# Kernel tuning notes

Hardware: AMD Instinct MI355X
Metric: run time of the kernel (lower is better)

Reference implementation:

```python
import jax, jax.numpy as jnp
import numpy as np

NUM_EXPERTS = 8
TOP_K = 2


def setup_inputs() -> dict:
    key = jax.random.key(0)
    k1, k2, k3, k4, k5 = jax.random.split(key, 5)
    H, F, E = 1024, 4096, NUM_EXPERTS
    s = 0.02
    return {
        "hidden_states": jax.random.normal(k1, (2, 2048, H), jnp.float32),
        "w_router": jax.random.normal(k2, (E, H), jnp.float32) * s,
        "w1": jax.random.normal(k3, (E, F, H), jnp.float32) * s,
        "w2": jax.random.normal(k4, (E, H, F), jnp.float32) * s,
        "w3": jax.random.normal(k5, (E, F, H), jnp.float32) * s,
    }


def reference(hidden_states, w_router, w1, w2, w3):
    B, S, H = hidden_states.shape
    x = hidden_states.reshape(-1, H)  # [T, H]
    T = x.shape[0]
    # router (nn.Linear, no bias): logits = x @ W^T
    router_logits = x @ w_router.T  # [T, E]
    probs = jax.nn.softmax(router_logits.astype(jnp.float32), axis=-1)
    top_w, top_e = jax.lax.top_k(probs, TOP_K)  # [T, K]
    top_w = top_w / jnp.sum(top_w, axis=-1, keepdims=True)
    top_w = top_w.astype(x.dtype)
    # dense per-token gate matrix [T, E]; zero where expert not selected
    gates = jnp.zeros((T, NUM_EXPERTS), x.dtype).at[
        jnp.arange(T)[:, None], top_e
    ].add(top_w)
    out = jnp.zeros_like(x)
    for e in range(NUM_EXPERTS):  # fixed small expert loop
        h = jax.nn.silu(x @ w1[e].T) * (x @ w3[e].T)  # [T, F]
        out = out + gates[:, e:e + 1] * (h @ w2[e].T)
    return out.reshape(B, S, H), router_logits
```

## Files before the change

kernel.cpp:

```cpp
#include <hip/hip_runtime.h>
#include <hip/hip_bf16.h>
#include <stdint.h>

#define T_TOK 4096
#define H_DIM 1024
#define F_DIM 4096
#define NE 8
#define MG_BLKS 40

typedef float    f32x4  __attribute__((ext_vector_type(4)));
typedef __bf16   bf16x8 __attribute__((ext_vector_type(8)));
typedef uint16_t u16x8  __attribute__((ext_vector_type(8)));

#define AS1 __attribute__((address_space(1)))
#define AS3 __attribute__((address_space(3)))

__device__ __forceinline__ uint16_t f2bf(float f) {
  return __builtin_bit_cast(uint16_t, __float2bfloat16(f));
}

__device__ __forceinline__ void gld16(const void* g, void* l) {
  __builtin_amdgcn_global_load_lds((const AS1 void*)g, (AS3 void*)l, 16, 0, 0);
}

__global__ __launch_bounds__(256) void router_k(
    const float* __restrict__ x, const float* __restrict__ wr,
    float* __restrict__ logits, uint16_t* __restrict__ xb,
    int* __restrict__ pairTok, float* __restrict__ pairGate,
    int* __restrict__ tokSlot, int* __restrict__ cnt)
{
  const int lane = threadIdx.x & 63;
  const int wid  = threadIdx.x >> 6;
  const int t    = blockIdx.x * 4 + wid;

  const float* xp = x + (size_t)t * H_DIM + lane * 16;
  f32x4 xv[4];
#pragma unroll
  for (int i = 0; i < 4; ++i) xv[i] = *(const f32x4*)(xp + 4 * i);

  u16x8 o0, o1;
#pragma unroll
  for (int j = 0; j < 4; ++j) {
    o0[j] = f2bf(xv[0][j]); o0[j + 4] = f2bf(xv[1][j]);
    o1[j] = f2bf(xv[2][j]); o1[j + 4] = f2bf(xv[3][j]);
  }
  uint16_t* xbp = xb + (size_t)t * H_DIM + lane * 16;
  *(u16x8*)xbp       = o0;
  *(u16x8*)(xbp + 8) = o1;

  float s[NE];
#pragma unroll
  for (int e = 0; e < NE; ++e) {
    const float* wp = wr + e * H_DIM + lane * 16;
    float acc = 0.f;
#pragma unroll
    for (int i = 0; i < 4; ++i) {
      f32x4 wv = *(const f32x4*)(wp + 4 * i);
#pragma unroll
      for (int j = 0; j < 4; ++j) acc += xv[i][j] * wv[j];
    }
#pragma unroll
    for (int off = 32; off > 0; off >>= 1) acc += __shfl_xor(acc, off, 64);
    s[e] = acc;
  }

  if (lane == 0) {
#pragma unroll
    for (int e = 0; e < NE; ++e) logits[t * NE + e] = s[e];
    int e1 = 0;
#pragma unroll
    for (int e = 1; e < NE; ++e) if (s[e] > s[e1]) e1 = e;
    int e2 = (e1 == 0) ? 1 : 0;
#pragma unroll
    for (int e = 0; e < NE; ++e)
      if (e != e1 && e != e2 && s[e] > s[e2]) e2 = e;
    const float d  = s[e2] - s[e1];
    const float g1 = 1.f / (1.f + __expf(d));
    const float g2 = 1.f - g1;
    int i1 = atomicAdd(cnt + e1, 1);
    pairTok[e1 * T_TOK + i1] = t;  pairGate[e1 * T_TOK + i1] = g1;
    int i2 = atomicAdd(cnt + e2, 1);
    pairTok[e2 * T_TOK + i2] = t;  pairGate[e2 * T_TOK + i2] = g2;
    int4 sl; sl.x = e1; sl.y = i1; sl.z = e2; sl.w = i2;
    ((int4*)tokSlot)[t] = sl;
  }
}

__global__ void prefix_k(const int* __restrict__ cnt, int* __restrict__ base) {
  if (threadIdx.x == 0) {
    int b = 0;
#pragma unroll
    for (int e = 0; e < NE; ++e) { base[e] = b; b += (cnt[e] + 255) & ~255; }
    base[NE] = b;
  }
}

__global__ __launch_bounds__(256, 2) void ffn1_k(
    const uint16_t* __restrict__ xb, const float* __restrict__ w1,
    const float* __restrict__ w3, uint16_t* __restrict__ hbuf,
    const int* __restrict__ pairTok, const float* __restrict__ pairGate,
    const int* __restrict__ cnt, const int* __restrict__ base)
{
  const int mg0 = blockIdx.y * 256;
  if (mg0 >= base[NE]) return;
  int e = 0;
#pragma unroll
  for (int k = 1; k < NE; ++k) if (mg0 >= base[k]) e = k;
  const int m0   = mg0 - base[e];
  const int cnte = cnt[e];
  const int n0   = blockIdx.x * 64;
  const int tid  = threadIdx.x;
  const int lane = tid & 63;
  const int wid  = tid >> 6;
  const int wm   = (wid >> 1) * 128;
  const int wn   = (wid & 1) * 32;

  __shared__ __align__(16) uint16_t lsA [256 * 64];
  __shared__ __align__(16) uint16_t lsB1[ 64 * 64];
  __shared__ __align__(16) uint16_t lsB3[ 64 * 64];
  __shared__ float lsG[256];

  {
    const int rr = m0 + tid;
    lsG[tid] = (rr < cnte) ? pairGate[e * T_TOK + rr] : 0.f;
  }

  const float* w1e = w1 + (size_t)e * F_DIM * H_DIM;
  const float* w3e = w3 + (size_t)e * F_DIM * H_DIM;

  const uint16_t* asrc[8];
#pragma unroll
  for (int q = 0; q < 8; ++q) {
    const int c = q * 256 + tid;
    const int row = c >> 3, pos = c & 7;
    const int kc  = pos ^ (row & 7);
    int ar = m0 + row; if (ar >= cnte) ar = cnte - 1;
    const int tok = pairTok[e * T_TOK + ar];
    asrc[q] = xb + (size_t)tok * H_DIM + kc * 8;
  }
  const float* b1src[2];
  const float* b3src[2];
  int bdst[2];
#pragma unroll
  for (int q = 0; q < 2; ++q) {
    const int c = q * 256 + tid;
    const int row = c >> 3, pos = c & 7;
    const int kc  = pos ^ (row & 7);
    bdst[q] = c * 8;
    b1src[q] = w1e + (size_t)(n0 + row) * H_DIM + kc * 8;
    b3src[q] = w3e + (size_t)(n0 + row) * H_DIM + kc * 8;
  }

  const f32x4 fz = {0.f, 0.f, 0.f, 0.f};
  f32x4 acc1[8][2], acc3[8][2];
#pragma unroll
  for (int i = 0; i < 8; ++i)
#pragma unroll
    for (int j = 0; j < 2; ++j) { acc1[i][j] = fz; acc3[i][j] = fz; }

  for (int kt = 0; kt < H_DIM; kt += 64) {
    __syncthreads();
#pragma unroll
    for (int q = 0; q < 8; ++q)
      gld16(asrc[q] + kt, &lsA[(q * 256 + tid) * 8]);
#pragma unroll
    for (int q = 0; q < 2; ++q) {
      const float* s1 = b1src[q] + kt;
      const float* s3 = b3src[q] + kt;
      f32x4 a0 = *(const f32x4*)s1;
      f32x4 a1 = *(const f32x4*)(s1 + 4);
      f32x4 c0 = *(const f32x4*)s3;
      f32x4 c1 = *(const f32x4*)(s3 + 4);
      u16x8 ob1, ob3;
#pragma unroll
      for (int j = 0; j < 4; ++j) {
        ob1[j] = f2bf(a0[j]); ob1[j + 4] = f2bf(a1[j]);
        ob3[j] = f2bf(c0[j]); ob3[j + 4] = f2bf(c1[j]);
      }
      *(u16x8*)&lsB1[bdst[q]] = ob1;
      *(u16x8*)&lsB3[bdst[q]] = ob3;
    }
    __syncthreads();
#pragma unroll
    for (int ks = 0; ks < 2; ++ks) {
      const int kg = ks * 4 + (lane >> 4);
      bf16x8 af[8], b1f[2], b3f[2];
#pragma unroll
      for (int i = 0; i < 8; ++i) {
        const int ar = wm + i * 16 + (lane & 15);
        af[i] = *(const bf16x8*)&lsA[ar * 64 + ((kg ^ (ar & 7)) * 8)];
      }
#pragma unroll
      for (int j = 0; j < 2; ++j) {
        const int br = wn + j * 16 + (lane & 15);
        b1f[j] = *(const bf16x8*)&lsB1[br * 64 + ((kg ^ (br & 7)) * 8)];
        b3f[j] = *(const bf16x8*)&lsB3[br * 64 + ((kg ^ (br & 7)) * 8)];
      }
#pragma unroll
      for (int i = 0; i < 8; ++i)
#pragma unroll
        for (int j = 0; j < 2; ++j) {
          acc1[i][j] = __builtin_amdgcn_mfma_f32_16x16x32_bf16(af[i], b1f[j], acc1[i][j], 0, 0, 0);
          acc3[i][j] = __builtin_amdgcn_mfma_f32_16x16x32_bf16(af[i], b3f[j], acc3[i][j], 0, 0, 0);
        }
    }
  }

  const int be = base[e];
#pragma unroll
  for (int i = 0; i < 8; ++i) {
#pragma unroll
    for (int r = 0; r < 4; ++r) {
      const int lrow = m0 + wm + i * 16 + (lane >> 4) * 4 + r;
      if (lrow < cnte) {
        const float g = lsG[lrow - m0];
        uint16_t* hp = hbuf + (size_t)(be + lrow) * F_DIM + n0 + wn + (lane & 15);
#pragma unroll
        for (int j = 0; j < 2; ++j) {
          const float a  = acc1[i][j][r];
          const float hv = g * (a / (1.f + __expf(-a))) * acc3[i][j][r];
          hp[j * 16] = f2bf(hv);
        }
      }
    }
  }
}

__global__ __launch_bounds__(256, 2) void ffn2_k(
    const uint16_t* __restrict__ hbuf, const float* __restrict__ w2,
    uint16_t* __restrict__ y, const int* __restrict__ cnt,
    const int* __restrict__ base)
{
  const int mg0 = blockIdx.y * 256;
  if (mg0 >= base[NE]) return;
  int e = 0;
#pragma unroll
  for (int k = 1; k < NE; ++k) if (mg0 >= base[k]) e = k;
  const int m0   = mg0 - base[e];
  const int cnte = cnt[e];
  const int n0   = blockIdx.x * 128;
  const int tid  = threadIdx.x;
  const int lane = tid & 63;
  const int wid  = tid >> 6;
  const int wm   = (wid >> 1) * 128;
  const int wn   = (wid & 1) * 64;

  __shared__ __align__(16) uint16_t lsA[256 * 64];
  __shared__ __align__(16) uint16_t lsB[128 * 64];

  const int be = base[e];
  const float* w2e = w2 + (size_t)e * H_DIM * F_DIM;

  const uint16_t* asrc[8];
#pragma unroll
  for (int q = 0; q < 8; ++q) {
    const int c = q * 256 + tid;
    const int row = c >> 3, pos = c & 7;
    const int kc  = pos ^ (row & 7);
    int rr = m0 + row; if (rr >= cnte) rr = cnte - 1;
    asrc[q] = hbuf + (size_t)(be + rr) * F_DIM + kc * 8;
  }
  const float* bsrc[4];
  int bdst[4];
#pragma unroll
  for (int q = 0; q < 4; ++q) {
    const int c = q * 256 + tid;
    const int row = c >> 3, pos = c & 7;
    const int kc  = pos ^ (row & 7);
    bdst[q] = c * 8;
    bsrc[q] = w2e + (size_t)(n0 + row) * F_DIM + kc * 8;
  }

  const f32x4 fz = {0.f, 0.f, 0.f, 0.f};
  f32x4 acc[8][4];
#pragma unroll
  for (int i = 0; i < 8; ++i)
#pragma unroll
    for (int j = 0; j < 4; ++j) acc[i][j] = fz;

  for (int kt = 0; kt < F_DIM; kt += 64) {
    __syncthreads();
#pragma unroll
    for (int q = 0; q < 8; ++q)
      gld16(asrc[q] + kt, &lsA[(q * 256 + tid) * 8]);
#pragma unroll
    for (int q = 0; q < 4; ++q) {
      const float* sb = bsrc[q] + kt;
      f32x4 b0 = *(const f32x4*)sb;
      f32x4 b1 = *(const f32x4*)(sb + 4);
      u16x8 ob;
#pragma unroll
      for (int j = 0; j < 4; ++j) { ob[j] = f2bf(b0[j]); ob[j + 4] = f2bf(b1[j]); }
      *(u16x8*)&lsB[bdst[q]] = ob;
    }
    __syncthreads();
#pragma unroll
    for (int ks = 0; ks < 2; ++ks) {
      const int kg = ks * 4 + (lane >> 4);
      bf16x8 af[8], bf[4];
#pragma unroll
      for (int i = 0; i < 8; ++i) {
        const int ar = wm + i * 16 + (lane & 15);
        af[i] = *(const bf16x8*)&lsA[ar * 64 + ((kg ^ (ar & 7)) * 8)];
      }
#pragma unroll
      for (int j = 0; j < 4; ++j) {
        const int br = wn + j * 16 + (lane & 15);
        bf[j] = *(const bf16x8*)&lsB[br * 64 + ((kg ^ (br & 7)) * 8)];
      }
#pragma unroll
      for (int i = 0; i < 8; ++i)
#pragma unroll
        for (int j = 0; j < 4; ++j)
          acc[i][j] = __builtin_amdgcn_mfma_f32_16x16x32_bf16(af[i], bf[j], acc[i][j], 0, 0, 0);
    }
  }

#pragma unroll
  for (int i = 0; i < 8; ++i) {
#pragma unroll
    for (int r = 0; r < 4; ++r) {
      const int lrow = m0 + wm + i * 16 + (lane >> 4) * 4 + r;
      if (lrow < cnte) {
        uint16_t* yp = y + (size_t)(be + lrow) * H_DIM + n0 + wn + (lane & 15);
#pragma unroll
        for (int j = 0; j < 4; ++j)
          yp[j * 16] = f2bf(acc[i][j][r]);
      }
    }
  }
}

__global__ __launch_bounds__(256) void combine_k(
    const uint16_t* __restrict__ y, const int* __restrict__ tokSlot,
    const int* __restrict__ base, float* __restrict__ out)
{
  const int t = blockIdx.x * 2 + (threadIdx.x >> 7);
  const int c = (threadIdx.x & 127) * 8;
  const int4 s = ((const int4*)tokSlot)[t];
  const uint16_t* y1 = y + (size_t)(base[s.x] + s.y) * H_DIM + c;
  const uint16_t* y2 = y + (size_t)(base[s.z] + s.w) * H_DIM + c;
  const u16x8 a = *(const u16x8*)y1;
  const u16x8 b = *(const u16x8*)y2;
  float* op = out + (size_t)t * H_DIM + c;
  f32x4 o0, o1;
#pragma unroll
  for (int j = 0; j < 4; ++j) {
    o0[j] = __bfloat162float(__hip_bfloat16_raw{a[j]}) +
            __bfloat162float(__hip_bfloat16_raw{b[j]});
    o1[j] = __bfloat162float(__hip_bfloat16_raw{a[j + 4]}) +
            __bfloat162float(__hip_bfloat16_raw{b[j + 4]});
  }
  *(f32x4*)op       = o0;
  *(f32x4*)(op + 4) = o1;
}

extern "C" void kernel_launch(void* const* d_in, const int* in_sizes, int n_in,
                              void* d_out, int out_size, void* d_ws, size_t ws_size,
                              hipStream_t stream)
{
  const float* x  = (const float*)d_in[0];
  const float* wr = (const float*)d_in[1];
  const float* w1 = (const float*)d_in[2];
  const float* w2 = (const float*)d_in[3];
  const float* w3 = (const float*)d_in[4];
  float* out    = (float*)d_out;
  float* logits = out + (size_t)T_TOK * H_DIM;

  uint8_t* ws = (uint8_t*)d_ws;
  const size_t PADROWS  = (size_t)MG_BLKS * 256;
  const size_t XB_OFF   = 0;
  const size_t HB_OFF   = XB_OFF + (size_t)T_TOK * H_DIM * 2;
  const size_t Y_OFF    = HB_OFF + PADROWS * F_DIM * 2;
  const size_t PT_OFF   = Y_OFF + PADROWS * H_DIM * 2;
  const size_t PG_OFF   = PT_OFF + (size_t)NE * T_TOK * 4;
  const size_t TS_OFF   = PG_OFF + (size_t)NE * T_TOK * 4;
  const size_t CNT_OFF  = TS_OFF + (size_t)T_TOK * 16;
  const size_t BASE_OFF = CNT_OFF + 64;
  const size_t NEED     = BASE_OFF + 64;
  if (ws_size < NEED) return;

  uint16_t* xb      = (uint16_t*)(ws + XB_OFF);
  uint16_t* hb      = (uint16_t*)(ws + HB_OFF);
  uint16_t* yb      = (uint16_t*)(ws + Y_OFF);
  int*      pairTok = (int*)(ws + PT_OFF);
  float*    pairGate= (float*)(ws + PG_OFF);
  int*      tokSlot = (int*)(ws + TS_OFF);
  int*      cnt     = (int*)(ws + CNT_OFF);
  int*      basep   = (int*)(ws + BASE_OFF);

  hipMemsetAsync(cnt, 0, 64, stream);
  router_k<<<T_TOK / 4, 256, 0, stream>>>(x, wr, logits, xb, pairTok, pairGate, tokSlot, cnt);
  prefix_k<<<1, 64, 0, stream>>>(cnt, basep);
  ffn1_k<<<dim3(F_DIM / 64, MG_BLKS, 1), 256, 0, stream>>>(xb, w1, w3, hb, pairTok, pairGate, cnt, basep);
  ffn2_k<<<dim3(H_DIM / 128, MG_BLKS, 1), 256, 0, stream>>>(hb, w2, yb, cnt, basep);
  combine_k<<<T_TOK / 2, 256, 0, stream>>>(yb, tokSlot, basep, out);
}
```

Baseline: 470.2 us.

## Pre-convert expert weights to bf16 and use direct-to-LDS bf16 GEMM kernels

Adds a vectorized fp32-to-bf16 conversion kernel that converts w1, w3 and w2 into workspace buffers on every call. New FFN kernels, ffn1b_k and ffn2b_k, then stream the bf16 weights straight into swizzled LDS with global_load_lds, with no in-kernel conversion. This halves weight bytes for each GEMM tile load and simplifies the loader. The cost is an extra full pass that reads the fp32 weights and writes the bf16 copies on every call, plus about 200MB of extra workspace. The code falls back to the old kernels when the workspace is too small.

```diff
diff --git a/kernel.cpp b/kernel.cpp
--- a/kernel.cpp
+++ b/kernel.cpp
@@ -21,6 +21,20 @@
 
 __device__ __forceinline__ void gld16(const void* g, void* l) {
   __builtin_amdgcn_global_load_lds((const AS1 void*)g, (AS3 void*)l, 16, 0, 0);
+}
+
+__global__ __launch_bounds__(256) void cvt_k(const float* __restrict__ src,
+                                             uint16_t* __restrict__ dst, int n8) {
+  const int stride = gridDim.x * blockDim.x;
+  for (int i = blockIdx.x * blockDim.x + threadIdx.x; i < n8; i += stride) {
+    const float* s = src + (size_t)i * 8;
+    f32x4 a = *(const f32x4*)s;
+    f32x4 b = *(const f32x4*)(s + 4);
+    u16x8 o;
+#pragma unroll
+    for (int j = 0; j < 4; ++j) { o[j] = f2bf(a[j]); o[j + 4] = f2bf(b[j]); }
+    *(u16x8*)(dst + (size_t)i * 8) = o;
+  }
 }
 
 __global__ __launch_bounds__(256) void router_k(
@@ -94,6 +108,221 @@
     base[NE] = b;
   }
 }
+
+
+__global__ __launch_bounds__(256, 2) void ffn1b_k(
+    const uint16_t* __restrict__ xb, const uint16_t* __restrict__ w1b,
+    const uint16_t* __restrict__ w3b, uint16_t* __restrict__ hbuf,
+    const int* __restrict__ pairTok, const float* __restrict__ pairGate,
+    const int* __restrict__ cnt, const int* __restrict__ base)
+{
+  const int mg0 = blockIdx.y * 256;
+  if (mg0 >= base[NE]) return;
+  int e = 0;
+#pragma unroll
+  for (int k = 1; k < NE; ++k) if (mg0 >= base[k]) e = k;
+  const int m0   = mg0 - base[e];
+  const int cnte = cnt[e];
+  const int n0   = blockIdx.x * 64;
+  const int tid  = threadIdx.x;
+  const int lane = tid & 63;
+  const int wid  = tid >> 6;
+  const int wm   = (wid >> 1) * 128;
+  const int wn   = (wid & 1) * 32;
+
+  __shared__ __align__(16) uint16_t lsA [256 * 64];
+  __shared__ __align__(16) uint16_t lsB1[ 64 * 64];
+  __shared__ __align__(16) uint16_t lsB3[ 64 * 64];
+  __shared__ float lsG[256];
+
+  {
+    const int rr = m0 + tid;
+    lsG[tid] = (rr < cnte) ? pairGate[e * T_TOK + rr] : 0.f;
+  }
+
+  const uint16_t* w1e = w1b + (size_t)e * F_DIM * H_DIM;
+  const uint16_t* w3e = w3b + (size_t)e * F_DIM * H_DIM;
+
+  const uint16_t* asrc[8];
+#pragma unroll
+  for (int q = 0; q < 8; ++q) {
+    const int c = q * 256 + tid;
+    const int row = c >> 3, pos = c & 7;
+    const int kc  = pos ^ (row & 7);
+    int ar = m0 + row; if (ar >= cnte) ar = cnte - 1;
+    const int tok = pairTok[e * T_TOK + ar];
+    asrc[q] = xb + (size_t)tok * H_DIM + kc * 8;
+  }
+  const uint16_t* b1src[2];
+  const uint16_t* b3src[2];
+#pragma unroll
+  for (int q = 0; q < 2; ++q) {
+    const int c = q * 256 + tid;
+    const int row = c >> 3, pos = c & 7;
+    const int kc  = pos ^ (row & 7);
+    b1src[q] = w1e + (size_t)(n0 + row) * H_DIM + kc * 8;
+    b3src[q] = w3e + (size_t)(n0 + row) * H_DIM + kc * 8;
+  }
+
+  const f32x4 fz = {0.f, 0.f, 0.f, 0.f};
+  f32x4 acc1[8][2], acc3[8][2];
+#pragma unroll
+  for (int i = 0; i < 8; ++i)
+#pragma unroll
+    for (int j = 0; j < 2; ++j) { acc1[i][j] = fz; acc3[i][j] = fz; }
+
+  for (int kt = 0; kt < H_DIM; kt += 64) {
+    __syncthreads();
+#pragma unroll
+    for (int q = 0; q < 8; ++q)
+      gld16(asrc[q] + kt, &lsA[(q * 256 + tid) * 8]);
+#pragma unroll
+    for (int q = 0; q < 2; ++q) {
+      gld16(b1src[q] + kt, &lsB1[(q * 256 + tid) * 8]);
+      gld16(b3src[q] + kt, &lsB3[(q * 256 + tid) * 8]);
+    }
+    __syncthreads();
+#pragma unroll
+    for (int ks = 0; ks < 2; ++ks) {
+      const int kg = ks * 4 + (lane >> 4);
+      bf16x8 af[8], b1f[2], b3f[2];
+#pragma unroll
+      for (int i = 0; i < 8; ++i) {
+        const int ar = wm + i * 16 + (lane & 15);
+        af[i] = *(const bf16x8*)&lsA[ar * 64 + ((kg ^ (ar & 7)) * 8)];
+      }
+#pragma unroll
+      for (int j = 0; j < 2; ++j) {
+        const int br = wn + j * 16 + (lane & 15);
+        b1f[j] = *(const bf16x8*)&lsB1[br * 64 + ((kg ^ (br & 7)) * 8)];
+        b3f[j] = *(const bf16x8*)&lsB3[br * 64 + ((kg ^ (br & 7)) * 8)];
+      }
+#pragma unroll
+      for (int i = 0; i < 8; ++i)
+#pragma unroll
+        for (int j = 0; j < 2; ++j) {
+          acc1[i][j] = __builtin_amdgcn_mfma_f32_16x16x32_bf16(af[i], b1f[j], acc1[i][j], 0, 0, 0);
+          acc3[i][j] = __builtin_amdgcn_mfma_f32_16x16x32_bf16(af[i], b3f[j], acc3[i][j], 0, 0, 0);
+        }
+    }
+  }
+
+  const int be = base[e];
+#pragma unroll
+  for (int i = 0; i < 8; ++i) {
+#pragma unroll
+    for (int r = 0; r < 4; ++r) {
+      const int lrow = m0 + wm + i * 16 + (lane >> 4) * 4 + r;
+      if (lrow < cnte) {
+        const float g = lsG[lrow - m0];
+        uint16_t* hp = hbuf + (size_t)(be + lrow) * F_DIM + n0 + wn + (lane & 15);
+#pragma unroll
+        for (int j = 0; j < 2; ++j) {
+          const float a  = acc1[i][j][r];
+          const float hv = g * (a / (1.f + __expf(-a))) * acc3[i][j][r];
+          hp[j * 16] = f2bf(hv);
+        }
+      }
+    }
+  }
+}
+
+__global__ __launch_bounds__(256, 2) void ffn2b_k(
+    const uint16_t* __restrict__ hbuf, const uint16_t* __restrict__ w2b,
+    uint16_t* __restrict__ y, const int* __restrict__ cnt,
+    const int* __restrict__ base)
+{
+  const int mg0 = blockIdx.y * 256;
+  if (mg0 >= base[NE]) return;
+  int e = 0;
+#pragma unroll
+  for (int k = 1; k < NE; ++k) if (mg0 >= base[k]) e = k;
+  const int m0   = mg0 - base[e];
+  const int cnte = cnt[e];
+  const int n0   = blockIdx.x * 128;
+  const int tid  = threadIdx.x;
+  const int lane = tid & 63;
+  const int wid  = tid >> 6;
+  const int wm   = (wid >> 1) * 128;
+  const int wn   = (wid & 1) * 64;
+
+  __shared__ __align__(16) uint16_t lsA[256 * 64];
+  __shared__ __align__(16) uint16_t lsB[128 * 64];
+
+  const int be = base[e];
+  const uint16_t* w2e = w2b + (size_t)e * H_DIM * F_DIM;
+
+  const uint16_t* asrc[8];
+#pragma unroll
+  for (int q = 0; q < 8; ++q) {
+    const int c = q * 256 + tid;
+    const int row = c >> 3, pos = c & 7;
+    const int kc  = pos ^ (row & 7);
+    int rr = m0 + row; if (rr >= cnte) rr = cnte - 1;
+    asrc[q] = hbuf + (size_t)(be + rr) * F_DIM + kc * 8;
+  }
+  const uint16_t* bsrc[4];
+#pragma unroll
+  for (int q = 0; q < 4; ++q) {
+    const int c = q * 256 + tid;
+    const int row = c >> 3, pos = c & 7;
+    const int kc  = pos ^ (row & 7);
+    bsrc[q] = w2e + (size_t)(n0 + row) * F_DIM + kc * 8;
+  }
+
+  const f32x4 fz = {0.f, 0.f, 0.f, 0.f};
+  f32x4 acc[8][4];
+#pragma unroll
+  for (int i = 0; i < 8; ++i)
+#pragma unroll
+    for (int j = 0; j < 4; ++j) acc[i][j] = fz;
+
+  for (int kt = 0; kt < F_DIM; kt += 64) {
+    __syncthreads();
+#pragma unroll
+    for (int q = 0; q < 8; ++q)
+      gld16(asrc[q] + kt, &lsA[(q * 256 + tid) * 8]);
+#pragma unroll
+    for (int q = 0; q < 4; ++q)
+      gld16(bsrc[q] + kt, &lsB[(q * 256 + tid) * 8]);
+    __syncthreads();
+#pragma unroll
+    for (int ks = 0; ks < 2; ++ks) {
+      const int kg = ks * 4 + (lane >> 4);
+      bf16x8 af[8], bf[4];
+#pragma unroll
+      for (int i = 0; i < 8; ++i) {
+        const int ar = wm + i * 16 + (lane & 15);
+        af[i] = *(const bf16x8*)&lsA[ar * 64 + ((kg ^ (ar & 7)) * 8)];
+      }
+#pragma unroll
+      for (int j = 0; j < 4; ++j) {
+        const int br = wn + j * 16 + (lane & 15);
+        bf[j] = *(const bf16x8*)&lsB[br * 64 + ((kg ^ (br & 7)) * 8)];
+      }
+#pragma unroll
+      for (int i = 0; i < 8; ++i)
+#pragma unroll
+        for (int j = 0; j < 4; ++j)
+          acc[i][j] = __builtin_amdgcn_mfma_f32_16x16x32_bf16(af[i], bf[j], acc[i][j], 0, 0, 0);
+    }
+  }
+
+#pragma unroll
+  for (int i = 0; i < 8; ++i) {
+#pragma unroll
+    for (int r = 0; r < 4; ++r) {
+      const int lrow = m0 + wm + i * 16 + (lane >> 4) * 4 + r;
+      if (lrow < cnte) {
+        uint16_t* yp = y + (size_t)(be + lrow) * H_DIM + n0 + wn + (lane & 15);
+#pragma unroll
+        for (int j = 0; j < 4; ++j)
+          yp[j * 16] = f2bf(acc[i][j][r]);
+      }
+    }
+  }
+}
+
 
 __global__ __launch_bounds__(256, 2) void ffn1_k(
     const uint16_t* __restrict__ xb, const float* __restrict__ w1,
@@ -369,6 +598,7 @@
 
   uint8_t* ws = (uint8_t*)d_ws;
   const size_t PADROWS  = (size_t)MG_BLKS * 256;
+  const size_t WELEMS   = (size_t)NE * F_DIM * H_DIM;
   const size_t XB_OFF   = 0;
   const size_t HB_OFF   = XB_OFF + (size_t)T_TOK * H_DIM * 2;
   const size_t Y_OFF    = HB_OFF + PADROWS * F_DIM * 2;
@@ -377,8 +607,12 @@
   const size_t TS_OFF   = PG_OFF + (size_t)NE * T_TOK * 4;
   const size_t CNT_OFF  = TS_OFF + (size_t)T_TOK * 16;
   const size_t BASE_OFF = CNT_OFF + 64;
-  const size_t NEED     = BASE_OFF + 64;
-  if (ws_size < NEED) return;
+  const size_t W1B_OFF  = (BASE_OFF + 64 + 255) & ~(size_t)255;
+  const size_t W3B_OFF  = W1B_OFF + WELEMS * 2;
+  const size_t W2B_OFF  = W3B_OFF + WELEMS * 2;
+  const size_t NEED_BIG = W2B_OFF + WELEMS * 2;
+  const size_t NEED_SM  = W1B_OFF;
+  if (ws_size < NEED_SM) return;
 
   uint16_t* xb      = (uint16_t*)(ws + XB_OFF);
   uint16_t* hb      = (uint16_t*)(ws + HB_OFF);
@@ -392,7 +626,20 @@
   hipMemsetAsync(cnt, 0, 64, stream);
   router_k<<<T_TOK / 4, 256, 0, stream>>>(x, wr, logits, xb, pairTok, pairGate, tokSlot, cnt);
   prefix_k<<<1, 64, 0, stream>>>(cnt, basep);
-  ffn1_k<<<dim3(F_DIM / 64, MG_BLKS, 1), 256, 0, stream>>>(xb, w1, w3, hb, pairTok, pairGate, cnt, basep);
-  ffn2_k<<<dim3(H_DIM / 128, MG_BLKS, 1), 256, 0, stream>>>(hb, w2, yb, cnt, basep);
+
+  if (ws_size >= NEED_BIG) {
+    uint16_t* w1b = (uint16_t*)(ws + W1B_OFF);
+    uint16_t* w3b = (uint16_t*)(ws + W3B_OFF);
+    uint16_t* w2b = (uint16_t*)(ws + W2B_OFF);
+    const int n8 = (int)(WELEMS / 8);
+    cvt_k<<<2048, 256, 0, stream>>>(w1, w1b, n8);
+    cvt_k<<<2048, 256, 0, stream>>>(w3, w3b, n8);
+    cvt_k<<<2048, 256, 0, stream>>>(w2, w2b, n8);
+    ffn1b_k<<<dim3(F_DIM / 64, MG_BLKS, 1), 256, 0, stream>>>(xb, w1b, w3b, hb, pairTok, pairGate, cnt, basep);
+    ffn2b_k<<<dim3(H_DIM / 128, MG_BLKS, 1), 256, 0, stream>>>(hb, w2b, yb, cnt, basep);
+  } else {
+    ffn1_k<<<dim3(F_DIM / 64, MG_BLKS, 1), 256, 0, stream>>>(xb, w1, w3, hb, pairTok, pairGate, cnt, basep);
+    ffn2_k<<<dim3(H_DIM / 128, MG_BLKS, 1), 256, 0, stream>>>(hb, w2, yb, cnt, basep);
+  }
   combine_k<<<T_TOK / 2, 256, 0, stream>>>(yb, tokSlot, basep, out);
 }
```

After: 525.2 us. +11.7%, slower.

## Double-buffer activation tiles and prefetch weight tiles in both FFN GEMMs

Applied to the files above, without the earlier changes.

Both expert GEMM kernels now double-buffer the activation LDS tile and prefetch the next fp32 weight tile into registers one iteration ahead. The fp32-to-bf16 conversion and LDS store happen after the compute barrier, so global load latency overlaps the MFMA work of the current tile. Wave priority is raised around the MFMA section. The per-block gate staging in LDS is dropped in favour of direct global reads in the epilogue. This costs more LDS (about 80 KB per block) and more registers, which could hurt occupancy or spill, and it relies on implicit vmcnt ordering to make sure the A-tile LDS writes have landed.

```diff
diff --git a/kernel.cpp b/kernel.cpp
--- a/kernel.cpp
+++ b/kernel.cpp
@@ -22,6 +22,8 @@
 __device__ __forceinline__ void gld16(const void* g, void* l) {
   __builtin_amdgcn_global_load_lds((const AS1 void*)g, (AS3 void*)l, 16, 0, 0);
 }
+
+#define FENCE() asm volatile("" ::: "memory")
 
 __global__ __launch_bounds__(256) void router_k(
     const float* __restrict__ x, const float* __restrict__ wr,
@@ -115,15 +117,9 @@
   const int wm   = (wid >> 1) * 128;
   const int wn   = (wid & 1) * 32;
 
-  __shared__ __align__(16) uint16_t lsA [256 * 64];
+  __shared__ __align__(16) uint16_t lsA [2][256 * 64];
   __shared__ __align__(16) uint16_t lsB1[ 64 * 64];
   __shared__ __align__(16) uint16_t lsB3[ 64 * 64];
-  __shared__ float lsG[256];
-
-  {
-    const int rr = m0 + tid;
-    lsG[tid] = (rr < cnte) ? pairGate[e * T_TOK + rr] : 0.f;
-  }
 
   const float* w1e = w1 + (size_t)e * F_DIM * H_DIM;
   const float* w3e = w3 + (size_t)e * F_DIM * H_DIM;
@@ -151,6 +147,31 @@
     b3src[q] = w3e + (size_t)(n0 + row) * H_DIM + kc * 8;
   }
 
+  f32x4 b1v[2][2], b3v[2][2];
+
+#define ISSUE_A1(buf, koff)                                               \
+  { _Pragma("unroll") for (int q = 0; q < 8; ++q)                         \
+      gld16(asrc[q] + (koff), &lsA[buf][(q * 256 + tid) * 8]); }
+
+#define LOAD_B1(koff)                                                     \
+  { _Pragma("unroll") for (int q = 0; q < 2; ++q) {                       \
+      b1v[q][0] = *(const f32x4*)(b1src[q] + (koff));                     \
+      b1v[q][1] = *(const f32x4*)(b1src[q] + (koff) + 4);                 \
+      b3v[q][0] = *(const f32x4*)(b3src[q] + (koff));                     \
+      b3v[q][1] = *(const f32x4*)(b3src[q] + (koff) + 4);                 \
+    } }
+
+#define CVTW_B1()                                                         \
+  { _Pragma("unroll") for (int q = 0; q < 2; ++q) {                       \
+      u16x8 ob1, ob3;                                                     \
+      _Pragma("unroll") for (int j = 0; j < 4; ++j) {                     \
+        ob1[j] = f2bf(b1v[q][0][j]); ob1[j + 4] = f2bf(b1v[q][1][j]);     \
+        ob3[j] = f2bf(b3v[q][0][j]); ob3[j + 4] = f2bf(b3v[q][1][j]);     \
+      }                                                                   \
+      *(u16x8*)&lsB1[bdst[q]] = ob1;                                      \
+      *(u16x8*)&lsB3[bdst[q]] = ob3;                                      \
+    } }
+
   const f32x4 fz = {0.f, 0.f, 0.f, 0.f};
   f32x4 acc1[8][2], acc3[8][2];
 #pragma unroll
@@ -158,29 +179,20 @@
 #pragma unroll
     for (int j = 0; j < 2; ++j) { acc1[i][j] = fz; acc3[i][j] = fz; }
 
-  for (int kt = 0; kt < H_DIM; kt += 64) {
-    __syncthreads();
-#pragma unroll
-    for (int q = 0; q < 8; ++q)
-      gld16(asrc[q] + kt, &lsA[(q * 256 + tid) * 8]);
-#pragma unroll
-    for (int q = 0; q < 2; ++q) {
-      const float* s1 = b1src[q] + kt;
-      const float* s3 = b3src[q] + kt;
-      f32x4 a0 = *(const f32x4*)s1;
-      f32x4 a1 = *(const f32x4*)(s1 + 4);
-      f32x4 c0 = *(const f32x4*)s3;
-      f32x4 c1 = *(const f32x4*)(s3 + 4);
-      u16x8 ob1, ob3;
-#pragma unroll
-      for (int j = 0; j < 4; ++j) {
-        ob1[j] = f2bf(a0[j]); ob1[j + 4] = f2bf(a1[j]);
-        ob3[j] = f2bf(c0[j]); ob3[j + 4] = f2bf(c1[j]);
-      }
-      *(u16x8*)&lsB1[bdst[q]] = ob1;
-      *(u16x8*)&lsB3[bdst[q]] = ob3;
-    }
-    __syncthreads();
+  const int NT = H_DIM / 64;
+  ISSUE_A1(0, 0)
+  LOAD_B1(0)
+  CVTW_B1()
+  ISSUE_A1(1, 64)
+  LOAD_B1(64)
+  FENCE();
+
+  for (int t = 0; t < NT; ++t) {
+    const int cur = t & 1;
+    asm volatile("s_waitcnt lgkmcnt(0)" ::: "memory");
+    __builtin_amdgcn_s_barrier();
+    FENCE();
+    __builtin_amdgcn_s_setprio(1);
 #pragma unroll
     for (int ks = 0; ks < 2; ++ks) {
       const int kg = ks * 4 + (lane >> 4);
@@ -188,7 +200,7 @@
 #pragma unroll
       for (int i = 0; i < 8; ++i) {
         const int ar = wm + i * 16 + (lane & 15);
-        af[i] = *(const bf16x8*)&lsA[ar * 64 + ((kg ^ (ar & 7)) * 8)];
+        af[i] = *(const bf16x8*)&lsA[cur][ar * 64 + ((kg ^ (ar & 7)) * 8)];
       }
 #pragma unroll
       for (int j = 0; j < 2; ++j) {
@@ -204,7 +216,21 @@
           acc3[i][j] = __builtin_amdgcn_mfma_f32_16x16x32_bf16(af[i], b3f[j], acc3[i][j], 0, 0, 0);
         }
     }
-  }
+    __builtin_amdgcn_s_setprio(0);
+    FENCE();
+    __builtin_amdgcn_s_barrier();
+    FENCE();
+    if (t + 1 < NT) {
+      CVTW_B1()
+      if (t + 2 < NT) {
+        ISSUE_A1(cur, (t + 2) * 64)
+        LOAD_B1((t + 2) * 64)
+      }
+    }
+  }
+#undef ISSUE_A1
+#undef LOAD_B1
+#undef CVTW_B1
 
   const int be = base[e];
 #pragma unroll
@@ -213,7 +239,7 @@
     for (int r = 0; r < 4; ++r) {
       const int lrow = m0 + wm + i * 16 + (lane >> 4) * 4 + r;
       if (lrow < cnte) {
-        const float g = lsG[lrow - m0];
+        const float g = pairGate[e * T_TOK + lrow];
         uint16_t* hp = hbuf + (size_t)(be + lrow) * F_DIM + n0 + wn + (lane & 15);
 #pragma unroll
         for (int j = 0; j < 2; ++j) {
@@ -245,7 +271,7 @@
   const int wm   = (wid >> 1) * 128;
   const int wn   = (wid & 1) * 64;
 
-  __shared__ __align__(16) uint16_t lsA[256 * 64];
+  __shared__ __align__(16) uint16_t lsA[2][256 * 64];
   __shared__ __align__(16) uint16_t lsB[128 * 64];
 
   const int be = base[e];
@@ -271,6 +297,27 @@
     bsrc[q] = w2e + (size_t)(n0 + row) * F_DIM + kc * 8;
   }
 
+  f32x4 bv[4][2];
+
+#define ISSUE_A2(buf, koff)                                               \
+  { _Pragma("unroll") for (int q = 0; q < 8; ++q)                         \
+      gld16(asrc[q] + (koff), &lsA[buf][(q * 256 + tid) * 8]); }
+
+#define LOAD_B2(koff)                                                     \
+  { _Pragma("unroll") for (int q = 0; q < 4; ++q) {                       \
+      bv[q][0] = *(const f32x4*)(bsrc[q] + (koff));                       \
+      bv[q][1] = *(const f32x4*)(bsrc[q] + (koff) + 4);                   \
+    } }
+
+#define CVTW_B2()                                                         \
+  { _Pragma("unroll") for (int q = 0; q < 4; ++q) {                       \
+      u16x8 ob;                                                           \
+      _Pragma("unroll") for (int j = 0; j < 4; ++j) {                     \
+        ob[j] = f2bf(bv[q][0][j]); ob[j + 4] = f2bf(bv[q][1][j]);         \
+      }                                                                   \
+      *(u16x8*)&lsB[bdst[q]] = ob;                                        \
+    } }
+
   const f32x4 fz = {0.f, 0.f, 0.f, 0.f};
   f32x4 acc[8][4];
 #pragma unroll
@@ -278,22 +325,20 @@
 #pragma unroll
     for (int j = 0; j < 4; ++j) acc[i][j] = fz;
 
-  for (int kt = 0; kt < F_DIM; kt += 64) {
-    __syncthreads();
-#pragma unroll
-    for (int q = 0; q < 8; ++q)
-      gld16(asrc[q] + kt, &lsA[(q * 256 + tid) * 8]);
-#pragma unroll
-    for (int q = 0; q < 4; ++q) {
-      const float* sb = bsrc[q] + kt;
-      f32x4 b0 = *(const f32x4*)sb;
-      f32x4 b1 = *(const f32x4*)(sb + 4);
-      u16x8 ob;
-#pragma unroll
-      for (int j = 0; j < 4; ++j) { ob[j] = f2bf(b0[j]); ob[j + 4] = f2bf(b1[j]); }
-      *(u16x8*)&lsB[bdst[q]] = ob;
-    }
-    __syncthreads();
+  const int NT = F_DIM / 64;
+  ISSUE_A2(0, 0)
+  LOAD_B2(0)
+  CVTW_B2()
+  ISSUE_A2(1, 64)
+  LOAD_B2(64)
+  FENCE();
+
+  for (int t = 0; t < NT; ++t) {
+    const int cur = t & 1;
+    asm volatile("s_waitcnt lgkmcnt(0)" ::: "memory");
+    __builtin_amdgcn_s_barrier();
+    FENCE();
+    __builtin_amdgcn_s_setprio(1);
 #pragma unroll
     for (int ks = 0; ks < 2; ++ks) {
       const int kg = ks * 4 + (lane >> 4);
@@ -301,7 +346,7 @@
 #pragma unroll
       for (int i = 0; i < 8; ++i) {
         const int ar = wm + i * 16 + (lane & 15);
-        af[i] = *(const bf16x8*)&lsA[ar * 64 + ((kg ^ (ar & 7)) * 8)];
+        af[i] = *(const bf16x8*)&lsA[cur][ar * 64 + ((kg ^ (ar & 7)) * 8)];
       }
 #pragma unroll
       for (int j = 0; j < 4; ++j) {
@@ -314,7 +359,21 @@
         for (int j = 0; j < 4; ++j)
           acc[i][j] = __builtin_amdgcn_mfma_f32_16x16x32_bf16(af[i], bf[j], acc[i][j], 0, 0, 0);
     }
-  }
+    __builtin_amdgcn_s_setprio(0);
+    FENCE();
+    __builtin_amdgcn_s_barrier();
+    FENCE();
+    if (t + 1 < NT) {
+      CVTW_B2()
+      if (t + 2 < NT) {
+        ISSUE_A2(cur, (t + 2) * 64)
+        LOAD_B2((t + 2) * 64)
+      }
+    }
+  }
+#undef ISSUE_A2
+#undef LOAD_B2
+#undef CVTW_B2
 
 #pragma unroll
   for (int i = 0; i < 8; ++i) {
```

After: 469.9 us. No clear change (-0.1%).

## Stage fp32 expert weights directly into LDS and convert to bf16 at fragment load

Applied to the files above, without the earlier changes.

The w1/w3/w2 tiles are now copied raw as fp32 into LDS with global_load_lds, replacing register loads followed by bf16 conversion and LDS stores. Conversion to bf16 moves to fragment-read time, using a new 16-way XOR swizzle for the fp32 layout. This removes the register round-trip and VGPR pressure of the weight staging path. The cost is double the LDS footprint for B tiles, which may lower occupancy (notably ffn2 with launch_bounds 2), plus repeated conversion work per fragment read. The gate value is also read from global memory in the epilogue instead of being staged in LDS.

```diff
diff --git a/kernel.cpp b/kernel.cpp
--- a/kernel.cpp
+++ b/kernel.cpp
@@ -21,6 +21,17 @@
 
 __device__ __forceinline__ void gld16(const void* g, void* l) {
   __builtin_amdgcn_global_load_lds((const AS1 void*)g, (AS3 void*)l, 16, 0, 0);
+}
+
+__device__ __forceinline__ bf16x8 ldsB_frag(const float* tile, int row, int kg) {
+  const int p0 = (2 * kg) ^ (row & 15);
+  const int p1 = (2 * kg + 1) ^ (row & 15);
+  const f32x4 v0 = *(const f32x4*)&tile[row * 64 + p0 * 4];
+  const f32x4 v1 = *(const f32x4*)&tile[row * 64 + p1 * 4];
+  u16x8 ub;
+#pragma unroll
+  for (int j = 0; j < 4; ++j) { ub[j] = f2bf(v0[j]); ub[j + 4] = f2bf(v1[j]); }
+  return __builtin_bit_cast(bf16x8, ub);
 }
 
 __global__ __launch_bounds__(256) void router_k(
@@ -116,14 +127,8 @@
   const int wn   = (wid & 1) * 32;
 
   __shared__ __align__(16) uint16_t lsA [256 * 64];
-  __shared__ __align__(16) uint16_t lsB1[ 64 * 64];
-  __shared__ __align__(16) uint16_t lsB3[ 64 * 64];
-  __shared__ float lsG[256];
-
-  {
-    const int rr = m0 + tid;
-    lsG[tid] = (rr < cnte) ? pairGate[e * T_TOK + rr] : 0.f;
-  }
+  __shared__ __align__(16) float    lsB1[ 64 * 64];
+  __shared__ __align__(16) float    lsB3[ 64 * 64];
 
   const float* w1e = w1 + (size_t)e * F_DIM * H_DIM;
   const float* w3e = w3 + (size_t)e * F_DIM * H_DIM;
@@ -138,17 +143,15 @@
     const int tok = pairTok[e * T_TOK + ar];
     asrc[q] = xb + (size_t)tok * H_DIM + kc * 8;
   }
-  const float* b1src[2];
-  const float* b3src[2];
-  int bdst[2];
-#pragma unroll
-  for (int q = 0; q < 2; ++q) {
+  const float* b1src[4];
+  const float* b3src[4];
+#pragma unroll
+  for (int q = 0; q < 4; ++q) {
     const int c = q * 256 + tid;
-    const int row = c >> 3, pos = c & 7;
-    const int kc  = pos ^ (row & 7);
-    bdst[q] = c * 8;
-    b1src[q] = w1e + (size_t)(n0 + row) * H_DIM + kc * 8;
-    b3src[q] = w3e + (size_t)(n0 + row) * H_DIM + kc * 8;
+    const int row = c >> 4, pos = c & 15;
+    const int kc  = pos ^ (row & 15);
+    b1src[q] = w1e + (size_t)(n0 + row) * H_DIM + kc * 4;
+    b3src[q] = w3e + (size_t)(n0 + row) * H_DIM + kc * 4;
   }
 
   const f32x4 fz = {0.f, 0.f, 0.f, 0.f};
@@ -164,21 +167,9 @@
     for (int q = 0; q < 8; ++q)
       gld16(asrc[q] + kt, &lsA[(q * 256 + tid) * 8]);
 #pragma unroll
-    for (int q = 0; q < 2; ++q) {
-      const float* s1 = b1src[q] + kt;
-      const float* s3 = b3src[q] + kt;
-      f32x4 a0 = *(const f32x4*)s1;
-      f32x4 a1 = *(const f32x4*)(s1 + 4);
-      f32x4 c0 = *(const f32x4*)s3;
-      f32x4 c1 = *(const f32x4*)(s3 + 4);
-      u16x8 ob1, ob3;
-#pragma unroll
-      for (int j = 0; j < 4; ++j) {
-        ob1[j] = f2bf(a0[j]); ob1[j + 4] = f2bf(a1[j]);
-        ob3[j] = f2bf(c0[j]); ob3[j + 4] = f2bf(c1[j]);
-      }
-      *(u16x8*)&lsB1[bdst[q]] = ob1;
-      *(u16x8*)&lsB3[bdst[q]] = ob3;
+    for (int q = 0; q < 4; ++q) {
+      gld16(b1src[q] + kt, &lsB1[(q * 256 + tid) * 4]);
+      gld16(b3src[q] + kt, &lsB3[(q * 256 + tid) * 4]);
     }
     __syncthreads();
 #pragma unroll
@@ -193,8 +184,8 @@
 #pragma unroll
       for (int j = 0; j < 2; ++j) {
         const int br = wn + j * 16 + (lane & 15);
-        b1f[j] = *(const bf16x8*)&lsB1[br * 64 + ((kg ^ (br & 7)) * 8)];
-        b3f[j] = *(const bf16x8*)&lsB3[br * 64 + ((kg ^ (br & 7)) * 8)];
+        b1f[j] = ldsB_frag(lsB1, br, kg);
+        b3f[j] = ldsB_frag(lsB3, br, kg);
       }
 #pragma unroll
       for (int i = 0; i < 8; ++i)
@@ -213,7 +204,7 @@
     for (int r = 0; r < 4; ++r) {
       const int lrow = m0 + wm + i * 16 + (lane >> 4) * 4 + r;
       if (lrow < cnte) {
-        const float g = lsG[lrow - m0];
+        const float g = pairGate[e * T_TOK + lrow];
         uint16_t* hp = hbuf + (size_t)(be + lrow) * F_DIM + n0 + wn + (lane & 15);
 #pragma unroll
         for (int j = 0; j < 2; ++j) {
@@ -246,7 +237,7 @@
   const int wn   = (wid & 1) * 64;
 
   __shared__ __align__(16) uint16_t lsA[256 * 64];
-  __shared__ __align__(16) uint16_t lsB[128 * 64];
+  __shared__ __align__(16) float    lsB[128 * 64];
 
   const int be = base[e];
   const float* w2e = w2 + (size_t)e * H_DIM * F_DIM;
@@ -260,15 +251,13 @@
     int rr = m0 + row; if (rr >= cnte) rr = cnte - 1;
     asrc[q] = hbuf + (size_t)(be + rr) * F_DIM + kc * 8;
   }
-  const float* bsrc[4];
-  int bdst[4];
-#pragma unroll
-  for (int q = 0; q < 4; ++q) {
+  const float* bsrc[8];
+#pragma unroll
+  for (int q = 0; q < 8; ++q) {
     const int c = q * 256 + tid;
-    const int row = c >> 3, pos = c & 7;
-    const int kc  = pos ^ (row & 7);
-    bdst[q] = c * 8;
-    bsrc[q] = w2e + (size_t)(n0 + row) * F_DIM + kc * 8;
+    const int row = c >> 4, pos = c & 15;
+    const int kc  = pos ^ (row & 15);
+    bsrc[q] = w2e + (size_t)(n0 + row) * F_DIM + kc * 4;
   }
 
   const f32x4 fz = {0.f, 0.f, 0.f, 0.f};
@@ -284,15 +273,8 @@
     for (int q = 0; q < 8; ++q)
       gld16(asrc[q] + kt, &lsA[(q * 256 + tid) * 8]);
 #pragma unroll
-    for (int q = 0; q < 4; ++q) {
-      const float* sb = bsrc[q] + kt;
-      f32x4 b0 = *(const f32x4*)sb;
-      f32x4 b1 = *(const f32x4*)(sb + 4);
-      u16x8 ob;
-#pragma unroll
-      for (int j = 0; j < 4; ++j) { ob[j] = f2bf(b0[j]); ob[j + 4] = f2bf(b1[j]); }
-      *(u16x8*)&lsB[bdst[q]] = ob;
-    }
+    for (int q = 0; q < 8; ++q)
+      gld16(bsrc[q] + kt, &lsB[(q * 256 + tid) * 4]);
     __syncthreads();
 #pragma unroll
     for (int ks = 0; ks < 2; ++ks) {
@@ -306,7 +288,7 @@
 #pragma unroll
       for (int j = 0; j < 4; ++j) {
         const int br = wn + j * 16 + (lane & 15);
-        bf[j] = *(const bf16x8*)&lsB[br * 64 + ((kg ^ (br & 7)) * 8)];
+        bf[j] = ldsB_frag(lsB, br, kg);
       }
 #pragma unroll
       for (int i = 0; i < 8; ++i)
```

After: 468.4 us. About the same (-0.4%).
